# Kernel tuning notes

Measured on AMD Instinct MI355X. Metric: run time of the kernel, lower is better.

## Reference

```python
import jax, jax.numpy as jnp
import numpy as np

K = 512      # num_embeddings
D = 64       # embedding_dim
N, H, W = 64, 64, 64


def setup_inputs() -> dict:
    key = jax.random.key(0)
    k1, k2 = jax.random.split(key)
    z_e = jax.random.normal(k1, (N, D, H, W), dtype=jnp.float32)
    # torch init: uniform_(-1/K, 1/K)
    emb_weight = jax.random.uniform(k2, (K, D), dtype=jnp.float32,
                                    minval=-1.0 / K, maxval=1.0 / K)
    return {"z_e": z_e, "emb_weight": emb_weight}


def reference(z_e, emb_weight):
    n, d, h, w = z_e.shape
    # (N, D, H, W) -> (N*H*W, D)
    z_flat = jnp.transpose(z_e, (0, 2, 3, 1)).reshape(-1, d)
    # squared L2 distances via ||z||^2 + ||e||^2 - 2 z.e
    z_sq = jnp.sum(z_flat * z_flat, axis=1, keepdims=True)        # (M, 1)
    e_sq = jnp.sum(emb_weight * emb_weight, axis=1)               # (K,)
    dots = z_flat @ emb_weight.T                                  # (M, K)
    distances = z_sq + e_sq - 2.0 * dots
    indices = jnp.argmin(distances, axis=1)                       # (M,)
    z_q_flat = emb_weight[indices]                                # gather (M, D)
    # vq loss: mse(stop_grad(z_e), z_q)
    diff = jax.lax.stop_gradient(z_flat) - z_q_flat
    vq_loss = jnp.mean(diff * diff)
    # straight-through estimator
    z_q_st = z_flat + jax.lax.stop_gradient(z_q_flat - z_flat)
    z_q = jnp.transpose(z_q_st.reshape(n, h, w, d), (0, 3, 1, 2))
    return z_q, vq_loss, indices.reshape(n, h, w)
```

## Files before the change

### kernel.cpp

```cpp
#include <hip/hip_runtime.h>

#define VQ_D   64
#define VQ_K   512
#define VQ_HW  4096
#define VQ_M   262144
#define VQ_LOSS_OFF 16777216
#define VQ_IDX_OFF  16777217

#define VQ_EPS  1e-4f

#define WS_CNT_OFF  8
#define WS_ESQ_OFF  12
#define WS_LIST_OFF 2060
#define WS_NEED     (2060 + 4 * VQ_M)

typedef float  f32x4  __attribute__((ext_vector_type(4)));
typedef short  bf16x8 __attribute__((ext_vector_type(8)));

__device__ __forceinline__ unsigned short f2bf_rne(float f) {
    unsigned u = __float_as_uint(f);
    u += 0x7FFFu + ((u >> 16) & 1u);
    return (unsigned short)(u >> 16);
}
__device__ __forceinline__ float bf2f(unsigned short h) {
    return __uint_as_float(((unsigned)h) << 16);
}
__device__ __forceinline__ int ldx(int slot) {
    return (slot << 4) ^ (((slot >> 4) & 3) << 4);
}

__global__ void vq_prep(const float* __restrict__ emb, float* __restrict__ esq) {
#pragma clang fp contract(off)
    int k = blockIdx.x * 256 + threadIdx.x;
    if (k < VQ_K) {
        const float* e = emb + k * VQ_D;
        float p[VQ_D];
#pragma unroll
        for (int d = 0; d < VQ_D; ++d) p[d] = e[d] * e[d];
        float r[8];
#pragma unroll
        for (int j = 0; j < 8; ++j) r[j] = p[j];
#pragma unroll
        for (int i = 8; i < VQ_D; i += 8)
#pragma unroll
            for (int j = 0; j < 8; ++j) r[j] += p[i + j];
        esq[k] = ((r[0] + r[1]) + (r[2] + r[3])) + ((r[4] + r[5]) + (r[6] + r[7]));
    }
}

__device__ __forceinline__ int vq_exact_point(
        const float* __restrict__ zr,
        const float* __restrict__ emb,
        const float* __restrict__ esq,
        int lane)
{
    float r8[8];
#pragma unroll
    for (int dj = 0; dj < 8; ++dj) {
        float f = zr[(size_t)dj * 4096];
        r8[dj] = f * f;
    }
#pragma unroll
    for (int i = 8; i < 64; i += 8)
#pragma unroll
        for (int dj = 0; dj < 8; ++dj) {
            float f = zr[(size_t)(i + dj) * 4096];
            r8[dj] += f * f;
        }
    const float zsq = ((r8[0] + r8[1]) + (r8[2] + r8[3]))
                    + ((r8[4] + r8[5]) + (r8[6] + r8[7]));
    float a[8];
#pragma unroll
    for (int q = 0; q < 8; ++q) a[q] = 0.f;
    const float* er0 = emb + (size_t)(lane * 8) * VQ_D;
    for (int c4 = 0; c4 < 16; ++c4) {
        f32x4 z4;
#pragma unroll
        for (int x = 0; x < 4; ++x) z4[x] = zr[(size_t)(c4 * 4 + x) * 4096];
#pragma unroll
        for (int q = 0; q < 8; ++q) {
            f32x4 e4 = *(const f32x4*)(er0 + q * VQ_D + c4 * 4);
#pragma unroll
            for (int x = 0; x < 4; ++x)
                a[q] = __builtin_fmaf(z4[x], e4[x], a[q]);
        }
    }
    float fb = 3.4e38f; int fk = 0;
#pragma unroll
    for (int q = 0; q < 8; ++q) {
        const int kk = lane * 8 + q;
        float tt = zsq + esq[kk];
        float dd = tt - 2.0f * a[q];
        if (dd < fb) { fb = dd; fk = kk; }
    }
#pragma unroll
    for (int off = 32; off > 0; off >>= 1) {
        float ob = __shfl_xor(fb, off, 64);
        int   ok = __shfl_xor(fk, off, 64);
        if (ob < fb || (ob == fb && ok < fk)) { fb = ob; fk = ok; }
    }
    return fk;
}

__global__ __launch_bounds__(256, 4) void vq_main_fast(
        const float* __restrict__ z_e,
        const float* __restrict__ emb,
        const float* __restrict__ esq,
        float* __restrict__ out,
        int* __restrict__ cnt_p,
        int* __restrict__ list)
{
#pragma clang fp contract(off)
    __shared__ __align__(16) char lbh[8192];
    __shared__ __align__(16) char lbl[8192];
    __shared__ float lesq[512];

    const int tid  = threadIdx.x;
    const int wave = tid >> 6, lane = tid & 63;
    const int c15  = lane & 15, g = lane >> 4;

    lesq[tid]       = esq[tid];
    lesq[tid + 256] = esq[tid + 256];

    const int mblk = blockIdx.x * 128;
    const int n    = mblk >> 12;
    const int hwb  = (mblk & 4095) + wave * 32;
    const float* zn = z_e + (size_t)n * 262144;

    bf16x8 ah[2][2], al[2][2];
#pragma unroll
    for (int ms = 0; ms < 2; ++ms) {
        const int hw = hwb + ms * 16 + c15;
#pragma unroll
        for (int s = 0; s < 2; ++s) {
#pragma unroll
            for (int e = 0; e < 8; ++e) {
                const int d = 32 * s + 8 * g + e;
                float f = zn[(size_t)d * 4096 + hw];
                unsigned short h = f2bf_rne(f);
                ah[ms][s][e] = (short)h;
                al[ms][s][e] = (short)f2bf_rne(f - bf2f(h));
            }
        }
    }

    float best[2][4], sec[2][4];
    int   bidx[2][4];
#pragma unroll
    for (int ms = 0; ms < 2; ++ms)
#pragma unroll
        for (int r = 0; r < 4; ++r) {
            best[ms][r] = 3.4e38f; sec[ms][r] = 3.4e38f; bidx[ms][r] = 0;
        }

    for (int ph = 0; ph < 8; ++ph) {
        __syncthreads();
#pragma unroll
        for (int j = 0; j < 2; ++j) {
            const int f8  = j * 256 + tid;
            const int row = f8 >> 3;
            const int ch  = f8 & 7;
            const float* src = emb + ((ph * 64 + row) * 64 + ch * 8);
            float x[8];
            *(f32x4*)&x[0] = *(const f32x4*)(src);
            *(f32x4*)&x[4] = *(const f32x4*)(src + 4);
            bf16x8 vh, vl;
#pragma unroll
            for (int e = 0; e < 8; ++e) {
                unsigned short h = f2bf_rne(x[e]);
                vh[e] = (short)h;
                vl[e] = (short)f2bf_rne(x[e] - bf2f(h));
            }
            const int s  = ch >> 2, gg = ch & 3;
            const int tl = row >> 4, cc = row & 15;
            const int slot = (tl * 2 + s) * 64 + gg * 16 + cc;
            *(bf16x8*)(lbh + ldx(slot)) = vh;
            *(bf16x8*)(lbl + ldx(slot)) = vl;
        }
        __syncthreads();

        bf16x8 cbh0 = *(const bf16x8*)(lbh + ldx(0 * 64 + lane));
        bf16x8 cbh1 = *(const bf16x8*)(lbh + ldx(1 * 64 + lane));
        bf16x8 cbl0 = *(const bf16x8*)(lbl + ldx(0 * 64 + lane));
        bf16x8 cbl1 = *(const bf16x8*)(lbl + ldx(1 * 64 + lane));
#pragma unroll
        for (int tl = 0; tl < 4; ++tl) {
            bf16x8 nbh0 = cbh0, nbh1 = cbh1, nbl0 = cbl0, nbl1 = cbl1;
            if (tl < 3) {
                nbh0 = *(const bf16x8*)(lbh + ldx((tl * 2 + 2) * 64 + lane));
                nbh1 = *(const bf16x8*)(lbh + ldx((tl * 2 + 3) * 64 + lane));
                nbl0 = *(const bf16x8*)(lbl + ldx((tl * 2 + 2) * 64 + lane));
                nbl1 = *(const bf16x8*)(lbl + ldx((tl * 2 + 3) * 64 + lane));
            }
            f32x4 acc0 = {0.f, 0.f, 0.f, 0.f};
            f32x4 acc1 = {0.f, 0.f, 0.f, 0.f};
            acc0 = __builtin_amdgcn_mfma_f32_16x16x32_bf16(ah[0][0], cbh0, acc0, 0, 0, 0);
            acc1 = __builtin_amdgcn_mfma_f32_16x16x32_bf16(ah[1][0], cbh0, acc1, 0, 0, 0);
            acc0 = __builtin_amdgcn_mfma_f32_16x16x32_bf16(ah[0][1], cbh1, acc0, 0, 0, 0);
            acc1 = __builtin_amdgcn_mfma_f32_16x16x32_bf16(ah[1][1], cbh1, acc1, 0, 0, 0);
            acc0 = __builtin_amdgcn_mfma_f32_16x16x32_bf16(al[0][0], cbh0, acc0, 0, 0, 0);
            acc1 = __builtin_amdgcn_mfma_f32_16x16x32_bf16(al[1][0], cbh0, acc1, 0, 0, 0);
            acc0 = __builtin_amdgcn_mfma_f32_16x16x32_bf16(al[0][1], cbh1, acc0, 0, 0, 0);
            acc1 = __builtin_amdgcn_mfma_f32_16x16x32_bf16(al[1][1], cbh1, acc1, 0, 0, 0);
            acc0 = __builtin_amdgcn_mfma_f32_16x16x32_bf16(ah[0][0], cbl0, acc0, 0, 0, 0);
            acc1 = __builtin_amdgcn_mfma_f32_16x16x32_bf16(ah[1][0], cbl0, acc1, 0, 0, 0);
            acc0 = __builtin_amdgcn_mfma_f32_16x16x32_bf16(ah[0][1], cbl1, acc0, 0, 0, 0);
            acc1 = __builtin_amdgcn_mfma_f32_16x16x32_bf16(ah[1][1], cbl1, acc1, 0, 0, 0);

            const int tg = ph * 4 + tl;
            const float ev = lesq[tg * 16 + c15];
            const int   k  = tg * 16 + c15;
#pragma unroll
            for (int r = 0; r < 4; ++r) {
                float v0 = __builtin_fmaf(-2.f, acc0[r], ev);
                bool lt0 = v0 < best[0][r];
                sec[0][r]  = lt0 ? best[0][r] : fminf(sec[0][r], v0);
                best[0][r] = lt0 ? v0 : best[0][r];
                bidx[0][r] = lt0 ? k : bidx[0][r];
                float v1 = __builtin_fmaf(-2.f, acc1[r], ev);
                bool lt1 = v1 < best[1][r];
                sec[1][r]  = lt1 ? best[1][r] : fminf(sec[1][r], v1);
                best[1][r] = lt1 ? v1 : best[1][r];
                bidx[1][r] = lt1 ? k : bidx[1][r];
            }
            cbh0 = nbh0; cbh1 = nbh1; cbl0 = nbl0; cbl1 = nbl1;
        }
    }

#pragma unroll
    for (int ms = 0; ms < 2; ++ms)
#pragma unroll
        for (int r = 0; r < 4; ++r) {
            float b = best[ms][r], s2 = sec[ms][r]; int bi = bidx[ms][r];
#pragma unroll
            for (int off = 1; off <= 8; off <<= 1) {
                float ob = __shfl_xor(b,  off, 64);
                float os = __shfl_xor(s2, off, 64);
                int   oi = __shfl_xor(bi, off, 64);
                bool lt = ob < b;
                float loser = lt ? b : ob;
                s2 = fminf(fminf(s2, os), loser);
                b  = lt ? ob : b;
                bi = lt ? oi : bi;
            }
            best[ms][r] = b; sec[ms][r] = s2; bidx[ms][r] = bi;
        }

    const int srcl = 16 * ((lane & 15) >> 2);
    float bb_ = 3.4e38f, ss_ = 3.4e38f; int ii_ = 0;
#pragma unroll
    for (int ms = 0; ms < 2; ++ms)
#pragma unroll
        for (int r = 0; r < 4; ++r) {
            float gb = __shfl(best[ms][r], srcl, 64);
            float gs = __shfl(sec[ms][r],  srcl, 64);
            int   gi = __shfl(bidx[ms][r], srcl, 64);
            bool hit = (ms == (lane >> 4)) && (r == (lane & 3));
            bb_ = hit ? gb : bb_; ss_ = hit ? gs : ss_; ii_ = hit ? gi : ii_;
        }
    const bool own = lane < 32;

    const int m_own = mblk + wave * 32 + lane;
    unsigned long long amb = __ballot(own && (ss_ - bb_ < VQ_EPS));
    const int nw = __popcll(amb);
    int base = 0;
    if (nw) {
        if (lane == 0) base = atomicAdd(cnt_p, nw);
        base = __shfl(base, 0, 64);
        if (own && (amb >> lane) & 1ull) {
            const int pos = __popcll(amb & ((1ull << lane) - 1ull));
            list[base + pos] = m_own;
        }
    }

    if (own)
        out[VQ_IDX_OFF + m_own] = (float)ii_;
}

__global__ __launch_bounds__(256, 4) void vq_rescue(
        const float* __restrict__ z_e,
        const float* __restrict__ emb,
        const float* __restrict__ esq,
        float* __restrict__ out,
        const int* __restrict__ cnt_p,
        const int* __restrict__ list)
{
#pragma clang fp contract(off)
    const int wave = threadIdx.x >> 6, lane = threadIdx.x & 63;
    const int gw = blockIdx.x * 4 + wave;
    const int nw = gridDim.x * 4;
    const int cnt = *cnt_p;
    for (int i = gw; i < cnt; i += nw) {
        const int m = list[i];
        const int n = m >> 12, hw = m & 4095;
        const float* zr = z_e + (size_t)n * 262144 + hw;
        const int fk = vq_exact_point(zr, emb, esq, lane);
        if (lane == 0) out[VQ_IDX_OFF + m] = (float)fk;
    }
}

__global__ __launch_bounds__(256, 4) void vq_main_fb(
        const float* __restrict__ z_e,
        const float* __restrict__ emb,
        const float* __restrict__ esq,
        float* __restrict__ out)
{
#pragma clang fp contract(off)
    __shared__ __align__(16) char lbh[16384];
    __shared__ __align__(16) char lbl[16384];
    __shared__ float lesq[512];

    const int tid  = threadIdx.x;
    const int wave = tid >> 6, lane = tid & 63;
    const int c15  = lane & 15, g = lane >> 4;

    lesq[tid]       = esq[tid];
    lesq[tid + 256] = esq[tid + 256];

    const int mblk = blockIdx.x * 128;
    const int n    = mblk >> 12;
    const int hwb  = (mblk & 4095) + wave * 32;
    const float* zn = z_e + (size_t)n * 262144;

    bf16x8 ah[2][2], al[2][2];
#pragma unroll
    for (int ms = 0; ms < 2; ++ms) {
        const int hw = hwb + ms * 16 + c15;
#pragma unroll
        for (int s = 0; s < 2; ++s) {
#pragma unroll
            for (int e = 0; e < 8; ++e) {
                const int d = 32 * s + 8 * g + e;
                float f = zn[(size_t)d * 4096 + hw];
                unsigned short h = f2bf_rne(f);
                ah[ms][s][e] = (short)h;
                al[ms][s][e] = (short)f2bf_rne(f - bf2f(h));
            }
        }
    }

    float best[2][4], sec[2][4];
    int   bidx[2][4];
#pragma unroll
    for (int ms = 0; ms < 2; ++ms)
#pragma unroll
        for (int r = 0; r < 4; ++r) {
            best[ms][r] = 3.4e38f; sec[ms][r] = 3.4e38f; bidx[ms][r] = 0;
        }

    for (int ph = 0; ph < 4; ++ph) {
        __syncthreads();
#pragma unroll
        for (int j = 0; j < 4; ++j) {
            const int f8  = j * 256 + tid;
            const int row = f8 >> 3;
            const int ch  = f8 & 7;
            const float* src = emb + ((ph * 128 + row) * 64 + ch * 8);
            float x[8];
            *(f32x4*)&x[0] = *(const f32x4*)(src);
            *(f32x4*)&x[4] = *(const f32x4*)(src + 4);
            bf16x8 vh, vl;
#pragma unroll
            for (int e = 0; e < 8; ++e) {
                unsigned short h = f2bf_rne(x[e]);
                vh[e] = (short)h;
                vl[e] = (short)f2bf_rne(x[e] - bf2f(h));
            }
            const int s  = ch >> 2, gg = ch & 3;
            const int tl = row >> 4, cc = row & 15;
            const int slot = (tl * 2 + s) * 64 + gg * 16 + cc;
            *(bf16x8*)(lbh + ldx(slot)) = vh;
            *(bf16x8*)(lbl + ldx(slot)) = vl;
        }
        __syncthreads();

        bf16x8 cbh0 = *(const bf16x8*)(lbh + ldx(0 * 64 + lane));
        bf16x8 cbh1 = *(const bf16x8*)(lbh + ldx(1 * 64 + lane));
        bf16x8 cbl0 = *(const bf16x8*)(lbl + ldx(0 * 64 + lane));
        bf16x8 cbl1 = *(const bf16x8*)(lbl + ldx(1 * 64 + lane));
#pragma unroll
        for (int tl = 0; tl < 8; ++tl) {
            bf16x8 nbh0 = cbh0, nbh1 = cbh1, nbl0 = cbl0, nbl1 = cbl1;
            if (tl < 7) {
                nbh0 = *(const bf16x8*)(lbh + ldx((tl * 2 + 2) * 64 + lane));
                nbh1 = *(const bf16x8*)(lbh + ldx((tl * 2 + 3) * 64 + lane));
                nbl0 = *(const bf16x8*)(lbl + ldx((tl * 2 + 2) * 64 + lane));
                nbl1 = *(const bf16x8*)(lbl + ldx((tl * 2 + 3) * 64 + lane));
            }
            f32x4 acc0 = {0.f, 0.f, 0.f, 0.f};
            f32x4 acc1 = {0.f, 0.f, 0.f, 0.f};
            acc0 = __builtin_amdgcn_mfma_f32_16x16x32_bf16(ah[0][0], cbh0, acc0, 0, 0, 0);
            acc1 = __builtin_amdgcn_mfma_f32_16x16x32_bf16(ah[1][0], cbh0, acc1, 0, 0, 0);
            acc0 = __builtin_amdgcn_mfma_f32_16x16x32_bf16(ah[0][1], cbh1, acc0, 0, 0, 0);
            acc1 = __builtin_amdgcn_mfma_f32_16x16x32_bf16(ah[1][1], cbh1, acc1, 0, 0, 0);
            acc0 = __builtin_amdgcn_mfma_f32_16x16x32_bf16(al[0][0], cbh0, acc0, 0, 0, 0);
            acc1 = __builtin_amdgcn_mfma_f32_16x16x32_bf16(al[1][0], cbh0, acc1, 0, 0, 0);
            acc0 = __builtin_amdgcn_mfma_f32_16x16x32_bf16(al[0][1], cbh1, acc0, 0, 0, 0);
            acc1 = __builtin_amdgcn_mfma_f32_16x16x32_bf16(al[1][1], cbh1, acc1, 0, 0, 0);
            acc0 = __builtin_amdgcn_mfma_f32_16x16x32_bf16(ah[0][0], cbl0, acc0, 0, 0, 0);
            acc1 = __builtin_amdgcn_mfma_f32_16x16x32_bf16(ah[1][0], cbl0, acc1, 0, 0, 0);
            acc0 = __builtin_amdgcn_mfma_f32_16x16x32_bf16(ah[0][1], cbl1, acc0, 0, 0, 0);
            acc1 = __builtin_amdgcn_mfma_f32_16x16x32_bf16(ah[1][1], cbl1, acc1, 0, 0, 0);

            const int tg = ph * 8 + tl;
            const float ev = lesq[tg * 16 + c15];
            const int   k  = tg * 16 + c15;
#pragma unroll
            for (int r = 0; r < 4; ++r) {
                float v0 = __builtin_fmaf(-2.f, acc0[r], ev);
                bool lt0 = v0 < best[0][r];
                sec[0][r]  = lt0 ? best[0][r] : fminf(sec[0][r], v0);
                best[0][r] = lt0 ? v0 : best[0][r];
                bidx[0][r] = lt0 ? k : bidx[0][r];
                float v1 = __builtin_fmaf(-2.f, acc1[r], ev);
                bool lt1 = v1 < best[1][r];
                sec[1][r]  = lt1 ? best[1][r] : fminf(sec[1][r], v1);
                best[1][r] = lt1 ? v1 : best[1][r];
                bidx[1][r] = lt1 ? k : bidx[1][r];
            }
            cbh0 = nbh0; cbh1 = nbh1; cbl0 = nbl0; cbl1 = nbl1;
        }
    }

#pragma unroll
    for (int ms = 0; ms < 2; ++ms)
#pragma unroll
        for (int r = 0; r < 4; ++r) {
            float b = best[ms][r], s2 = sec[ms][r]; int bi = bidx[ms][r];
#pragma unroll
            for (int off = 1; off <= 8; off <<= 1) {
                float ob = __shfl_xor(b,  off, 64);
                float os = __shfl_xor(s2, off, 64);
                int   oi = __shfl_xor(bi, off, 64);
                bool lt = ob < b;
                float loser = lt ? b : ob;
                s2 = fminf(fminf(s2, os), loser);
                b  = lt ? ob : b;
                bi = lt ? oi : bi;
            }
            best[ms][r] = b; sec[ms][r] = s2; bidx[ms][r] = bi;
        }

    const int srcl = 16 * ((lane & 15) >> 2);
    float bb_ = 3.4e38f, ss_ = 3.4e38f; int ii_ = 0;
#pragma unroll
    for (int ms = 0; ms < 2; ++ms)
#pragma unroll
        for (int r = 0; r < 4; ++r) {
            float gb = __shfl(best[ms][r], srcl, 64);
            float gs = __shfl(sec[ms][r],  srcl, 64);
            int   gi = __shfl(bidx[ms][r], srcl, 64);
            bool hit = (ms == (lane >> 4)) && (r == (lane & 3));
            bb_ = hit ? gb : bb_; ss_ = hit ? gs : ss_; ii_ = hit ? gi : ii_;
        }
    const bool own = lane < 32;

    unsigned long long msk = __ballot(own && (ss_ - bb_ < VQ_EPS));
    while (msk) {
        const int j = __ffsll(msk) - 1;
        msk &= msk - 1;
        const int fk = vq_exact_point(zn + hwb + j, emb, lesq, lane);
        if (lane == j) ii_ = fk;
    }

    if (own)
        out[VQ_IDX_OFF + mblk + wave * 32 + lane] = (float)ii_;
}

__global__ __launch_bounds__(256, 8) void vq_epi(
        const float* __restrict__ z_e,
        const float* __restrict__ emb,
        float* __restrict__ out,
        double* __restrict__ loss_acc)
{
#pragma clang fp contract(off)
    __shared__ float wsum[4];
    const int tid  = threadIdx.x;
    const int wave = tid >> 6, lane = tid & 63;
    const int m    = blockIdx.x * 256 + tid;
    const int n    = m >> 12;
    const int hw   = m & 4095;

    const float* zp = z_e + (size_t)n * 262144 + hw;
    const int ii = (int)out[VQ_IDX_OFF + m];
    const float* eb = emb + (size_t)ii * VQ_D;
    float* op = out + (size_t)n * 262144 + hw;

    float lsum = 0.f;
#pragma unroll
    for (int c4 = 0; c4 < 16; ++c4) {
        f32x4 e4 = *(const f32x4*)(eb + c4 * 4);
#pragma unroll
        for (int x = 0; x < 4; ++x) {
            const int d = c4 * 4 + x;
            float q = e4[x];
            op[(size_t)d * 4096] = q;
            float diff = zp[(size_t)d * 4096] - q;
            lsum = __builtin_fmaf(diff, diff, lsum);
        }
    }

    for (int off = 32; off > 0; off >>= 1)
        lsum += __shfl_down(lsum, off, 64);
    if (lane == 0) wsum[wave] = lsum;
    __syncthreads();
    if (tid == 0) {
        float b = wsum[0] + wsum[1] + wsum[2] + wsum[3];
        atomicAdd(loss_acc, (double)b);
    }
}

__global__ void vq_fin(const double* __restrict__ loss_acc, float* __restrict__ out) {
    if (threadIdx.x == 0)
        out[VQ_LOSS_OFF] = (float)(*loss_acc / 16777216.0);
}

extern "C" void kernel_launch(void* const* d_in, const int* in_sizes, int n_in,
                              void* d_out, int out_size, void* d_ws, size_t ws_size,
                              hipStream_t stream) {
    const float* z_e = (const float*)d_in[0];
    const float* emb = (const float*)d_in[1];
    float* out = (float*)d_out;
    char* wsb = (char*)d_ws;

    double* loss_acc = (double*)wsb;

    if (ws_size >= (size_t)WS_NEED) {
        float* esq = (float*)(wsb + WS_ESQ_OFF);
        int*   cnt = (int*)(wsb + WS_CNT_OFF);
        int*   lst = (int*)(wsb + WS_LIST_OFF);
        (void)hipMemsetAsync(d_ws, 0, 12, stream);
        vq_prep<<<2, 256, 0, stream>>>(emb, esq);
        vq_main_fast<<<VQ_M / 128, 256, 0, stream>>>(z_e, emb, esq, out, cnt, lst);
        vq_rescue<<<256, 256, 0, stream>>>(z_e, emb, esq, out, cnt, lst);
        vq_epi<<<VQ_M / 256, 256, 0, stream>>>(z_e, emb, out, loss_acc);
        vq_fin<<<1, 64, 0, stream>>>(loss_acc, out);
    } else {
        float* esq = (float*)(wsb + 8);
        (void)hipMemsetAsync(d_ws, 0, 8, stream);
        vq_prep<<<2, 256, 0, stream>>>(emb, esq);
        vq_main_fb<<<VQ_M / 128, 256, 0, stream>>>(z_e, emb, esq, out);
        vq_epi<<<VQ_M / 256, 256, 0, stream>>>(z_e, emb, out, loss_acc);
        vq_fin<<<1, 64, 0, stream>>>(loss_acc, out);
    }
}
```

Baseline: 328.4 us.

## Use per-point adaptive ambiguity threshold and LDS-staged rescue kernel

The fast pass now computes an estimate of each point's squared norm and derives an ambiguity threshold from the float ulp scale of the distance, replacing the fixed epsilon. This aims to send fewer points to the exact rescue pass. The rescue kernel is rewritten to stage the whole transposed codebook and its squared norms in LDS with 512-thread blocks, so each wave handles one point with 8 codes per lane and a shuffle argmin, instead of calling the prior per-point helper. The adaptive threshold risks missing near-ties if the error bound is too tight, and the 128KB+ LDS footprint limits rescue occupancy to one block per CU.

```diff
diff --git a/kernel.cpp b/kernel.cpp
--- a/kernel.cpp
+++ b/kernel.cpp
@@ -128,20 +128,26 @@
     const float* zn = z_e + (size_t)n * 262144;
 
     bf16x8 ah[2][2], al[2][2];
+    float zsq_est[2];
 #pragma unroll
     for (int ms = 0; ms < 2; ++ms) {
         const int hw = hwb + ms * 16 + c15;
+        float sq = 0.f;
 #pragma unroll
         for (int s = 0; s < 2; ++s) {
 #pragma unroll
             for (int e = 0; e < 8; ++e) {
                 const int d = 32 * s + 8 * g + e;
                 float f = zn[(size_t)d * 4096 + hw];
+                sq = __builtin_fmaf(f, f, sq);
                 unsigned short h = f2bf_rne(f);
                 ah[ms][s][e] = (short)h;
                 al[ms][s][e] = (short)f2bf_rne(f - bf2f(h));
             }
         }
+        sq += __shfl_xor(sq, 16, 64);
+        sq += __shfl_xor(sq, 32, 64);
+        zsq_est[ms] = sq;
     }
 
     float best[2][4], sec[2][4];
@@ -260,8 +266,13 @@
         }
     const bool own = lane < 32;
 
+    const float zq   = (lane & 16) ? zsq_est[1] : zsq_est[0];
+    const float t_ub = zq * 1.0001f + 0.501f;
+    const float p2   = __uint_as_float((__float_as_uint(t_ub) >> 23) << 23);
+    const float eps  = p2 * 2.3841858e-7f + 1.6e-5f;
+
     const int m_own = mblk + wave * 32 + lane;
-    unsigned long long amb = __ballot(own && (ss_ - bb_ < VQ_EPS));
+    unsigned long long amb = __ballot(own && (ss_ - bb_ < eps));
     const int nw = __popcll(amb);
     int base = 0;
     if (nw) {
@@ -277,7 +288,7 @@
         out[VQ_IDX_OFF + m_own] = (float)ii_;
 }
 
-__global__ __launch_bounds__(256, 4) void vq_rescue(
+__global__ __launch_bounds__(512, 1) void vq_rescue(
         const float* __restrict__ z_e,
         const float* __restrict__ emb,
         const float* __restrict__ esq,
@@ -286,15 +297,59 @@
         const int* __restrict__ list)
 {
 #pragma clang fp contract(off)
-    const int wave = threadIdx.x >> 6, lane = threadIdx.x & 63;
-    const int gw = blockIdx.x * 4 + wave;
-    const int nw = gridDim.x * 4;
+    __shared__ float lt[64 * 512];
+    __shared__ float lesq[512];
+
+    const int tid = threadIdx.x, wave = tid >> 6, lane = tid & 63;
+    lesq[tid] = esq[tid];
+#pragma unroll
+    for (int i = 0; i < 16; ++i) {
+        f32x4 v = *(const f32x4*)(emb + tid * 64 + i * 4);
+#pragma unroll
+        for (int x = 0; x < 4; ++x) lt[(i * 4 + x) * 512 + tid] = v[x];
+    }
+    __syncthreads();
+
     const int cnt = *cnt_p;
-    for (int i = gw; i < cnt; i += nw) {
+    const int nw  = gridDim.x * 8;
+    for (int i = blockIdx.x * 8 + wave; i < cnt; i += nw) {
         const int m = list[i];
         const int n = m >> 12, hw = m & 4095;
         const float* zr = z_e + (size_t)n * 262144 + hw;
-        const int fk = vq_exact_point(zr, emb, esq, lane);
+        float zf[64];
+#pragma unroll
+        for (int d = 0; d < 64; ++d) zf[d] = zr[(size_t)d * 4096];
+        float r8[8];
+#pragma unroll
+        for (int j = 0; j < 8; ++j) r8[j] = zf[j] * zf[j];
+#pragma unroll
+        for (int ii = 8; ii < 64; ii += 8)
+#pragma unroll
+            for (int j = 0; j < 8; ++j) r8[j] += zf[ii + j] * zf[ii + j];
+        const float zsq = ((r8[0] + r8[1]) + (r8[2] + r8[3]))
+                        + ((r8[4] + r8[5]) + (r8[6] + r8[7]));
+        float a[8];
+#pragma unroll
+        for (int q = 0; q < 8; ++q) a[q] = 0.f;
+#pragma unroll
+        for (int d = 0; d < 64; ++d)
+#pragma unroll
+            for (int q = 0; q < 8; ++q)
+                a[q] = __builtin_fmaf(zf[d], lt[d * 512 + lane + 64 * q], a[q]);
+        float fb = 3.4e38f; int fk = 0;
+#pragma unroll
+        for (int q = 0; q < 8; ++q) {
+            const int kk = lane + 64 * q;
+            float tt = zsq + lesq[kk];
+            float dd = tt - 2.0f * a[q];
+            if (dd < fb) { fb = dd; fk = kk; }
+        }
+#pragma unroll
+        for (int off = 32; off > 0; off >>= 1) {
+            float ob = __shfl_xor(fb, off, 64);
+            int   ok = __shfl_xor(fk, off, 64);
+            if (ob < fb || (ob == fb && ok < fk)) { fb = ob; fk = ok; }
+        }
         if (lane == 0) out[VQ_IDX_OFF + m] = (float)fk;
     }
 }
@@ -532,7 +587,7 @@
         (void)hipMemsetAsync(d_ws, 0, 12, stream);
         vq_prep<<<2, 256, 0, stream>>>(emb, esq);
         vq_main_fast<<<VQ_M / 128, 256, 0, stream>>>(z_e, emb, esq, out, cnt, lst);
-        vq_rescue<<<256, 256, 0, stream>>>(z_e, emb, esq, out, cnt, lst);
+        vq_rescue<<<256, 512, 0, stream>>>(z_e, emb, esq, out, cnt, lst);
         vq_epi<<<VQ_M / 256, 256, 0, stream>>>(z_e, emb, out, loss_acc);
         vq_fin<<<1, 64, 0, stream>>>(loss_acc, out);
     } else {
```

Result: no change. 328.9 us (+0.2%).
